# Optimization experiments

Hardware: AMD Instinct MI355X
Metric: run time of the kernel (lower is better)

## Reference

```python
import jax, jax.numpy as jnp
import numpy as np

B, T, C, H, WIN = 1, 2048, 512, 8, 48
DH = C // H  # 64


def setup_inputs() -> dict:
    key = jax.random.key(0)
    kx, kq, ko, kp = jax.random.split(key, 4)
    x = jax.random.normal(kx, (B, T, C), dtype=jnp.float32)
    W_qkv = jax.random.normal(kq, (C, 3 * C), dtype=jnp.float32) / np.sqrt(C).astype(np.float32)
    W_out = jax.random.normal(ko, (C, C), dtype=jnp.float32) / np.sqrt(C).astype(np.float32)
    # one random cycle permutation per head: perms[h, pi_pos] = original_pos
    perms = jax.vmap(lambda k: jax.random.permutation(k, T))(jax.random.split(kp, H)).astype(jnp.int32)
    return {"x": x, "W_qkv": W_qkv, "W_out": W_out, "perms": perms}


def _head_attn(qh, kh, vh, perm):
    # qh, kh, vh: [B, T, DH]; perm: [T] with perm[pi_pos] = original_pos
    Tn = perm.shape[0]
    inv_perm = jnp.argsort(perm)  # inv_perm[orig_pos] = pi_pos
    q_pi = qh[:, perm]
    k_pi = kh[:, perm]
    v_pi = vh[:, perm]
    offs = jnp.arange(-WIN, WIN + 1)                      # [W]
    pi_idx = jnp.arange(Tn)[:, None] + offs[None, :]      # [T, W]
    idx = jnp.clip(pi_idx, 0, Tn - 1)
    k_win = k_pi[:, idx]                                  # [B, T, W, DH]
    v_win = v_pi[:, idx]                                  # [B, T, W, DH]
    scores = jnp.einsum('btd,btwd->btw', q_pi, k_win) / np.sqrt(DH).astype(np.float32)
    neigh_orig = perm[idx]                                # [T, W] original positions of neighbors
    mask = (neigh_orig <= perm[:, None]) & (pi_idx >= 0) & (pi_idx < Tn)  # causal + window validity
    scores = jnp.where(mask[None], scores, jnp.finfo(scores.dtype).min)
    w = jax.nn.softmax(scores, axis=-1)                   # [B, T, W]
    y_pi = jnp.einsum('btw,btwd->btd', w, v_win)          # [B, T, DH]
    return y_pi[:, inv_perm]                              # back to original order


def reference(x, W_qkv, W_out, perms):
    qkv = x @ W_qkv                                       # [B, T, 3C]
    q, k, v = jnp.split(qkv, 3, axis=-1)
    q = q.reshape(B, T, H, DH)
    k = k.reshape(B, T, H, DH)
    v = v.reshape(B, T, H, DH)
    # heads are independent; vmap over head axis with per-head permutation
    y = jax.vmap(_head_attn, in_axes=(2, 2, 2, 0), out_axes=2)(q, k, v, perms)  # [B, T, H, DH]
    return y.reshape(B, T, C) @ W_out
```

## Files before the change

kernel.cpp:

```cpp
#include <hip/hip_runtime.h>
#include <float.h>
#include <math.h>

#define T_DIM 2048
#define C_DIM 512
#define QKV_LD 1536
#define NBLK 512

typedef float f32x4 __attribute__((ext_vector_type(4)));
typedef short s16x8 __attribute__((ext_vector_type(8)));

__device__ __forceinline__ unsigned short f2bf(float f) {
  unsigned u = __float_as_uint(f);
  return (unsigned short)((u + 0x7fffu + ((u >> 16) & 1u)) >> 16);
}

__device__ __forceinline__ void load16_to_lds(const void* g, void* l) {
  __builtin_amdgcn_global_load_lds(
      (const __attribute__((address_space(1))) unsigned int*)g,
      (__attribute__((address_space(3))) unsigned int*)(unsigned int)(unsigned long long)l,
      16, 0, 0);
}

template <int BM, bool AF32, bool OUT16>
__device__ __forceinline__ void gemm_body(const void* __restrict__ Ap,
                                          const float* __restrict__ B,
                                          void* __restrict__ Cp,
                                          int N, int K, int tilesX,
                                          unsigned short* lA, unsigned short* lB,
                                          int tid, int bid) {
  constexpr int BK = 32;
  constexpr int BM2 = BM / 2, BN2 = 32;
  constexpr int MT = BM2 / 16, NT = 2;
  const int lane = tid & 63, w = tid >> 6, wr = w >> 1, wc = w & 1;
  const int fm = lane & 15, q4 = lane >> 4, q8 = q4 * 8;

  const int m0 = (bid / tilesX) * BM, n0 = (bid % tilesX) * 64;
  const int bn = lane;
  const int bslot = w ^ ((bn >> 1) & 3);

  f32x4 acc[MT][NT] = {};
  for (int k0 = 0; k0 < K; k0 += BK) {
    __syncthreads();
    if constexpr (AF32) {
      const float* A = (const float*)Ap;
#pragma unroll
      for (int i = 0; i < BM / 64; ++i) {
        int c = i * 256 + tid;
        int row = c >> 2, c8 = (c & 3) * 8;
        const float* src = &A[(size_t)(m0 + row) * K + k0 + c8];
        float4 v0 = *(const float4*)src;
        float4 v1 = *(const float4*)(src + 4);
        uint4 o;
        o.x = f2bf(v0.x) | ((unsigned)f2bf(v0.y) << 16);
        o.y = f2bf(v0.z) | ((unsigned)f2bf(v0.w) << 16);
        o.z = f2bf(v1.x) | ((unsigned)f2bf(v1.y) << 16);
        o.w = f2bf(v1.z) | ((unsigned)f2bf(v1.w) << 16);
        *(uint4*)(lA + row * 32 + c8) = o;
      }
    } else {
      const unsigned short* A = (const unsigned short*)Ap;
#pragma unroll
      for (int i = 0; i < BM / 64; ++i) {
        int c = i * 256 + tid, row = c >> 2, c8 = (c & 3) * 8;
        load16_to_lds(&A[(size_t)(m0 + row) * K + k0 + c8], lA + c * 8);
      }
    }
    {
      float f[8];
#pragma unroll
      for (int i = 0; i < 8; ++i)
        f[i] = B[(size_t)(k0 + w * 8 + i) * N + n0 + bn];
      uint4 o;
      o.x = f2bf(f[0]) | ((unsigned)f2bf(f[1]) << 16);
      o.y = f2bf(f[2]) | ((unsigned)f2bf(f[3]) << 16);
      o.z = f2bf(f[4]) | ((unsigned)f2bf(f[5]) << 16);
      o.w = f2bf(f[6]) | ((unsigned)f2bf(f[7]) << 16);
      *(uint4*)(lB + bn * 32 + bslot * 8) = o;
    }
    __syncthreads();
    s16x8 a[MT], b[NT];
#pragma unroll
    for (int mi = 0; mi < MT; ++mi)
      a[mi] = *(const s16x8*)&lA[(wr * BM2 + mi * 16 + fm) * BK + q8];
#pragma unroll
    for (int ni = 0; ni < NT; ++ni) {
      int row = wc * BN2 + ni * 16 + fm;
      b[ni] = *(const s16x8*)&lB[row * 32 + ((q4 ^ ((row >> 1) & 3)) * 8)];
    }
#pragma unroll
    for (int mi = 0; mi < MT; ++mi)
#pragma unroll
      for (int ni = 0; ni < NT; ++ni)
        acc[mi][ni] = __builtin_amdgcn_mfma_f32_16x16x32_bf16(a[mi], b[ni], acc[mi][ni], 0, 0, 0);
  }
#pragma unroll
  for (int mi = 0; mi < MT; ++mi)
#pragma unroll
    for (int ni = 0; ni < NT; ++ni)
#pragma unroll
      for (int r = 0; r < 4; ++r) {
        int row = m0 + wr * BM2 + mi * 16 + q4 * 4 + r;
        int col = n0 + wc * BN2 + ni * 16 + fm;
        if constexpr (OUT16)
          ((unsigned short*)Cp)[(size_t)row * N + col] = f2bf(acc[mi][ni][r]);
        else
          ((float*)Cp)[(size_t)row * N + col] = acc[mi][ni][r];
      }
}

__global__ __launch_bounds__(256) void gemm1_kernel(const float* __restrict__ x,
                                                    const float* __restrict__ Wqkv,
                                                    unsigned short* __restrict__ qkvbf) {
  __shared__ __align__(16) unsigned short smem[(128 + 64) * 32];
  gemm_body<128, true, true>(x, Wqkv, qkvbf, QKV_LD, C_DIM, 24,
                             smem, smem + 128 * 32, threadIdx.x, blockIdx.x);
}
__global__ __launch_bounds__(256) void gemm2_kernel(const unsigned short* __restrict__ Ybf,
                                                    const float* __restrict__ Wout,
                                                    float* __restrict__ out) {
  __shared__ __align__(16) unsigned short smem[(64 + 64) * 32];
  gemm_body<64, false, false>(Ybf, Wout, out, C_DIM, C_DIM, 8,
                              smem, smem + 64 * 32, threadIdx.x, blockIdx.x);
}

__global__ __launch_bounds__(256) void attn_kernel(const unsigned short* __restrict__ qkvbf,
                                                   const int* __restrict__ perms,
                                                   unsigned short* __restrict__ Ybf) {
  __shared__ __align__(16) unsigned char smem[48768];
  int* ow            = (int*)smem;
  unsigned short* lQ = (unsigned short*)(smem + 512);
  unsigned short* lK = (unsigned short*)(smem + 5120);
  float* Sb          = (float*)(smem + 23552);
  unsigned short* lP = (unsigned short*)(smem + 40064);
  unsigned short* lVT= (unsigned short*)(smem + 5120);

  const int tid = threadIdx.x, bid = blockIdx.x;
  const int lane = tid & 63, w = tid >> 6;
  const int fm = lane & 15, q8 = (lane >> 4) * 8, q4 = lane >> 4;
  const int h = bid >> 6;
  const int t0 = (bid & 63) << 5;

  if (tid < 128) {
    int pi = t0 - 48 + tid;
    int idx = min(max(pi, 0), T_DIM - 1);
    ow[tid] = perms[h * T_DIM + idx];
  }
  __syncthreads();

#pragma unroll
  for (int it = 0; it < 4; ++it) {
    int c = it * 256 + tid;
    int row = c >> 3, k8 = c & 7;
    uint4 d = *(const uint4*)(qkvbf + (size_t)ow[row] * QKV_LD + C_DIM + h * 64 + k8 * 8);
    *(uint4*)(lK + row * 72 + k8 * 8) = d;
  }
  {
    int row = tid >> 3, k8 = tid & 7;
    uint4 d = *(const uint4*)(qkvbf + (size_t)ow[48 + row] * QKV_LD + h * 64 + k8 * 8);
    *(uint4*)(lQ + row * 72 + k8 * 8) = d;
  }
  __syncthreads();

  {
    f32x4 accs[2][2] = {};
#pragma unroll
    for (int kt = 0; kt < 2; ++kt) {
      s16x8 aq[2];
#pragma unroll
      for (int mi = 0; mi < 2; ++mi)
        aq[mi] = *(const s16x8*)&lQ[(mi * 16 + fm) * 72 + kt * 32 + q8];
#pragma unroll
      for (int ni = 0; ni < 2; ++ni) {
        s16x8 bk = *(const s16x8*)&lK[(w * 32 + ni * 16 + fm) * 72 + kt * 32 + q8];
#pragma unroll
        for (int mi = 0; mi < 2; ++mi)
          accs[mi][ni] = __builtin_amdgcn_mfma_f32_16x16x32_bf16(aq[mi], bk, accs[mi][ni], 0, 0, 0);
      }
    }
#pragma unroll
    for (int mi = 0; mi < 2; ++mi)
#pragma unroll
      for (int ni = 0; ni < 2; ++ni)
#pragma unroll
        for (int r = 0; r < 4; ++r)
          Sb[(mi * 16 + q4 * 4 + r) * 129 + w * 32 + ni * 16 + fm] = accs[mi][ni][r] * 0.125f;
  }
  __syncthreads();

#pragma unroll
  for (int it = 0; it < 4; ++it) {
    int c = it * 256 + tid;
    int j = c >> 3, d0 = (c & 7) * 8;
    uint4 v = *(const uint4*)(qkvbf + (size_t)ow[j] * QKV_LD + 2 * C_DIM + h * 64 + d0);
    lVT[(d0 + 0) * 136 + j] = (unsigned short)(v.x & 0xffff);
    lVT[(d0 + 1) * 136 + j] = (unsigned short)(v.x >> 16);
    lVT[(d0 + 2) * 136 + j] = (unsigned short)(v.y & 0xffff);
    lVT[(d0 + 3) * 136 + j] = (unsigned short)(v.y >> 16);
    lVT[(d0 + 4) * 136 + j] = (unsigned short)(v.z & 0xffff);
    lVT[(d0 + 5) * 136 + j] = (unsigned short)(v.z >> 16);
    lVT[(d0 + 6) * 136 + j] = (unsigned short)(v.w & 0xffff);
    lVT[(d0 + 7) * 136 + j] = (unsigned short)(v.w >> 16);
  }

  for (int si = 0; si < 8; ++si) {
    const int s = w * 8 + si;
    const int p = ow[48 + s];
    const int c1 = lane + 64;
    const float v0 = Sb[s * 129 + lane];
    const float v1 = Sb[s * 129 + c1];
    const int pi0 = t0 - 48 + lane;
    const bool valid0 = (lane >= s) && (pi0 >= 0) && (pi0 < T_DIM) && (ow[lane] <= p);
    const bool valid1 = (lane <= s + 32) && (pi0 + 64 < T_DIM) && (ow[c1] <= p);
    float mx = fmaxf(valid0 ? v0 : -FLT_MAX, valid1 ? v1 : -FLT_MAX);
#pragma unroll
    for (int off = 32; off > 0; off >>= 1) mx = fmaxf(mx, __shfl_xor(mx, off, 64));
    const float e0 = valid0 ? __expf(v0 - mx) : 0.f;
    const float e1 = valid1 ? __expf(v1 - mx) : 0.f;
    float sum = e0 + e1;
#pragma unroll
    for (int off = 32; off > 0; off >>= 1) sum += __shfl_xor(sum, off, 64);
    const float inv = 1.f / sum;
    lP[s * 136 + lane] = valid0 ? f2bf(e0 * inv) : (unsigned short)0;
    lP[s * 136 + c1]   = valid1 ? f2bf(e1 * inv) : (unsigned short)0;
  }
  __syncthreads();

  {
    const int wr = w >> 1, wc = w & 1;
    f32x4 acco[2] = {};
#pragma unroll
    for (int kt = 0; kt < 4; ++kt) {
      s16x8 ap = *(const s16x8*)&lP[(wr * 16 + fm) * 136 + kt * 32 + q8];
#pragma unroll
      for (int ni = 0; ni < 2; ++ni) {
        s16x8 bv = *(const s16x8*)&lVT[((wc * 2 + ni) * 16 + fm) * 136 + kt * 32 + q8];
        acco[ni] = __builtin_amdgcn_mfma_f32_16x16x32_bf16(ap, bv, acco[ni], 0, 0, 0);
      }
    }
#pragma unroll
    for (int ni = 0; ni < 2; ++ni)
#pragma unroll
      for (int r = 0; r < 4; ++r) {
        int q = wr * 16 + q4 * 4 + r;
        int d = (wc * 2 + ni) * 16 + fm;
        Ybf[(size_t)ow[48 + q] * C_DIM + h * 64 + d] = f2bf(acco[ni][r]);
      }
  }
}

extern "C" void kernel_launch(void* const* d_in, const int* in_sizes, int n_in,
                              void* d_out, int out_size, void* d_ws, size_t ws_size,
                              hipStream_t stream) {
  const float* x     = (const float*)d_in[0];
  const float* Wqkv  = (const float*)d_in[1];
  const float* Wout  = (const float*)d_in[2];
  const int*   perms = (const int*)d_in[3];
  float* out = (float*)d_out;
  unsigned short* ws = (unsigned short*)d_ws;

  unsigned short* qkvbf = ws;
  unsigned short* Ybf   = qkvbf + 3145728;

  gemm1_kernel<<<384, 256, 0, stream>>>(x, Wqkv, qkvbf);
  attn_kernel<<<NBLK, 256, 0, stream>>>(qkvbf, perms, Ybf);
  gemm2_kernel<<<256, 256, 0, stream>>>(Ybf, Wout, out);
}
```

Baseline: 104.6 us.

## Stage full weight K-panel in LDS once and prefetch A in GEMMs

Both GEMM kernels now convert the whole 512-deep bf16 B panel for their 64 output columns into LDS up front, using an XOR swizzle, rather than reloading and converting a 32-row slice every K step. gemm1 also prefetches the next fp32 A tile into registers while the current tile is in use. Separately, the attention V-transpose staging packs pairs of rows into 32-bit LDS stores, halving the number of scattered 16-bit writes. The cost is 64KB of LDS per GEMM block, which lowers occupancy, plus a long serial prologue before the first MFMA.

```diff
diff --git a/kernel.cpp b/kernel.cpp
--- a/kernel.cpp
+++ b/kernel.cpp
@@ -22,106 +22,140 @@
       16, 0, 0);
 }
 
-template <int BM, bool AF32, bool OUT16>
-__device__ __forceinline__ void gemm_body(const void* __restrict__ Ap,
-                                          const float* __restrict__ B,
-                                          void* __restrict__ Cp,
-                                          int N, int K, int tilesX,
-                                          unsigned short* lA, unsigned short* lB,
-                                          int tid, int bid) {
-  constexpr int BK = 32;
-  constexpr int BM2 = BM / 2, BN2 = 32;
-  constexpr int MT = BM2 / 16, NT = 2;
-  const int lane = tid & 63, w = tid >> 6, wr = w >> 1, wc = w & 1;
-  const int fm = lane & 15, q4 = lane >> 4, q8 = q4 * 8;
-
-  const int m0 = (bid / tilesX) * BM, n0 = (bid % tilesX) * 64;
-  const int bn = lane;
-  const int bslot = w ^ ((bn >> 1) & 3);
-
-  f32x4 acc[MT][NT] = {};
-  for (int k0 = 0; k0 < K; k0 += BK) {
-    __syncthreads();
-    if constexpr (AF32) {
-      const float* A = (const float*)Ap;
-#pragma unroll
-      for (int i = 0; i < BM / 64; ++i) {
-        int c = i * 256 + tid;
-        int row = c >> 2, c8 = (c & 3) * 8;
-        const float* src = &A[(size_t)(m0 + row) * K + k0 + c8];
-        float4 v0 = *(const float4*)src;
-        float4 v1 = *(const float4*)(src + 4);
-        uint4 o;
-        o.x = f2bf(v0.x) | ((unsigned)f2bf(v0.y) << 16);
-        o.y = f2bf(v0.z) | ((unsigned)f2bf(v0.w) << 16);
-        o.z = f2bf(v1.x) | ((unsigned)f2bf(v1.y) << 16);
-        o.w = f2bf(v1.z) | ((unsigned)f2bf(v1.w) << 16);
-        *(uint4*)(lA + row * 32 + c8) = o;
-      }
-    } else {
-      const unsigned short* A = (const unsigned short*)Ap;
-#pragma unroll
-      for (int i = 0; i < BM / 64; ++i) {
-        int c = i * 256 + tid, row = c >> 2, c8 = (c & 3) * 8;
-        load16_to_lds(&A[(size_t)(m0 + row) * K + k0 + c8], lA + c * 8);
-      }
-    }
-    {
-      float f[8];
-#pragma unroll
-      for (int i = 0; i < 8; ++i)
-        f[i] = B[(size_t)(k0 + w * 8 + i) * N + n0 + bn];
-      uint4 o;
-      o.x = f2bf(f[0]) | ((unsigned)f2bf(f[1]) << 16);
-      o.y = f2bf(f[2]) | ((unsigned)f2bf(f[3]) << 16);
-      o.z = f2bf(f[4]) | ((unsigned)f2bf(f[5]) << 16);
-      o.w = f2bf(f[6]) | ((unsigned)f2bf(f[7]) << 16);
-      *(uint4*)(lB + bn * 32 + bslot * 8) = o;
-    }
-    __syncthreads();
-    s16x8 a[MT], b[NT];
-#pragma unroll
-    for (int mi = 0; mi < MT; ++mi)
-      a[mi] = *(const s16x8*)&lA[(wr * BM2 + mi * 16 + fm) * BK + q8];
-#pragma unroll
-    for (int ni = 0; ni < NT; ++ni) {
-      int row = wc * BN2 + ni * 16 + fm;
-      b[ni] = *(const s16x8*)&lB[row * 32 + ((q4 ^ ((row >> 1) & 3)) * 8)];
-    }
-#pragma unroll
-    for (int mi = 0; mi < MT; ++mi)
-#pragma unroll
-      for (int ni = 0; ni < NT; ++ni)
-        acc[mi][ni] = __builtin_amdgcn_mfma_f32_16x16x32_bf16(a[mi], b[ni], acc[mi][ni], 0, 0, 0);
-  }
-#pragma unroll
-  for (int mi = 0; mi < MT; ++mi)
-#pragma unroll
-    for (int ni = 0; ni < NT; ++ni)
-#pragma unroll
-      for (int r = 0; r < 4; ++r) {
-        int row = m0 + wr * BM2 + mi * 16 + q4 * 4 + r;
-        int col = n0 + wc * BN2 + ni * 16 + fm;
-        if constexpr (OUT16)
-          ((unsigned short*)Cp)[(size_t)row * N + col] = f2bf(acc[mi][ni][r]);
-        else
-          ((float*)Cp)[(size_t)row * N + col] = acc[mi][ni][r];
-      }
+__device__ __forceinline__ void stage_B_panel(const float* __restrict__ W, int ldw,
+                                              int n0, unsigned short* lB,
+                                              int lane, int w) {
+  const int n = n0 + lane;
+#pragma unroll
+  for (int ko = 0; ko < 16; ++ko) {
+    const int chunk = ko * 4 + w;
+    const int kbase = chunk * 8;
+    float f[8];
+#pragma unroll
+    for (int j = 0; j < 8; ++j)
+      f[j] = W[(size_t)(kbase + j) * ldw + n];
+    uint4 o;
+    o.x = f2bf(f[0]) | ((unsigned)f2bf(f[1]) << 16);
+    o.y = f2bf(f[2]) | ((unsigned)f2bf(f[3]) << 16);
+    o.z = f2bf(f[4]) | ((unsigned)f2bf(f[5]) << 16);
+    o.w = f2bf(f[6]) | ((unsigned)f2bf(f[7]) << 16);
+    const int slot = chunk ^ (lane & 7);
+    *(uint4*)(lB + lane * 512 + slot * 8) = o;
+  }
 }
 
 __global__ __launch_bounds__(256) void gemm1_kernel(const float* __restrict__ x,
                                                     const float* __restrict__ Wqkv,
                                                     unsigned short* __restrict__ qkvbf) {
-  __shared__ __align__(16) unsigned short smem[(128 + 64) * 32];
-  gemm_body<128, true, true>(x, Wqkv, qkvbf, QKV_LD, C_DIM, 24,
-                             smem, smem + 128 * 32, threadIdx.x, blockIdx.x);
-}
+  __shared__ __align__(16) unsigned short lB[64 * 512];
+  __shared__ __align__(16) unsigned short lA[128 * 32];
+  const int tid = threadIdx.x, bid = blockIdx.x;
+  const int lane = tid & 63, w = tid >> 6, wr = w >> 1, wc = w & 1;
+  const int fm = lane & 15, q4 = lane >> 4, q8 = q4 * 8;
+  const int m0 = (bid / 24) * 128, n0 = (bid % 24) * 64;
+
+  stage_B_panel(Wqkv, QKV_LD, n0, lB, lane, w);
+
+  const int a_row = tid >> 2, a_c8 = (tid & 3) * 8;
+  const int a_row2 = a_row + 64;
+  float4 g[4];
+  auto loadA = [&](int kk) {
+    const float* s0 = &x[(size_t)(m0 + a_row) * C_DIM + kk + a_c8];
+    const float* s1 = &x[(size_t)(m0 + a_row2) * C_DIM + kk + a_c8];
+    g[0] = *(const float4*)s0; g[1] = *(const float4*)(s0 + 4);
+    g[2] = *(const float4*)s1; g[3] = *(const float4*)(s1 + 4);
+  };
+  loadA(0);
+
+  f32x4 acc[4][2] = {};
+  for (int i = 0; i < 16; ++i) {
+    __syncthreads();
+#pragma unroll
+    for (int ii = 0; ii < 2; ++ii) {
+      float4 v0 = g[ii * 2], v1 = g[ii * 2 + 1];
+      uint4 o;
+      o.x = f2bf(v0.x) | ((unsigned)f2bf(v0.y) << 16);
+      o.y = f2bf(v0.z) | ((unsigned)f2bf(v0.w) << 16);
+      o.z = f2bf(v1.x) | ((unsigned)f2bf(v1.y) << 16);
+      o.w = f2bf(v1.z) | ((unsigned)f2bf(v1.w) << 16);
+      *(uint4*)(lA + (ii ? a_row2 : a_row) * 32 + a_c8) = o;
+    }
+    __syncthreads();
+    if (i < 15) loadA((i + 1) * 32);
+
+    s16x8 a[4], b[2];
+#pragma unroll
+    for (int mi = 0; mi < 4; ++mi)
+      a[mi] = *(const s16x8*)&lA[(wr * 64 + mi * 16 + fm) * 32 + q8];
+#pragma unroll
+    for (int ni = 0; ni < 2; ++ni) {
+      int n = wc * 32 + ni * 16 + fm;
+      int slot = (i * 4 + q4) ^ (n & 7);
+      b[ni] = *(const s16x8*)&lB[n * 512 + slot * 8];
+    }
+#pragma unroll
+    for (int mi = 0; mi < 4; ++mi)
+#pragma unroll
+      for (int ni = 0; ni < 2; ++ni)
+        acc[mi][ni] = __builtin_amdgcn_mfma_f32_16x16x32_bf16(a[mi], b[ni], acc[mi][ni], 0, 0, 0);
+  }
+#pragma unroll
+  for (int mi = 0; mi < 4; ++mi)
+#pragma unroll
+    for (int ni = 0; ni < 2; ++ni)
+#pragma unroll
+      for (int r = 0; r < 4; ++r) {
+        int row = m0 + wr * 64 + mi * 16 + q4 * 4 + r;
+        int col = n0 + wc * 32 + ni * 16 + fm;
+        qkvbf[(size_t)row * QKV_LD + col] = f2bf(acc[mi][ni][r]);
+      }
+}
+
 __global__ __launch_bounds__(256) void gemm2_kernel(const unsigned short* __restrict__ Ybf,
                                                     const float* __restrict__ Wout,
                                                     float* __restrict__ out) {
-  __shared__ __align__(16) unsigned short smem[(64 + 64) * 32];
-  gemm_body<64, false, false>(Ybf, Wout, out, C_DIM, C_DIM, 8,
-                              smem, smem + 64 * 32, threadIdx.x, blockIdx.x);
+  __shared__ __align__(16) unsigned short lB[64 * 512];
+  __shared__ __align__(16) unsigned short lA[64 * 32];
+  const int tid = threadIdx.x, bid = blockIdx.x;
+  const int lane = tid & 63, w = tid >> 6, wr = w >> 1, wc = w & 1;
+  const int fm = lane & 15, q4 = lane >> 4, q8 = q4 * 8;
+  const int m0 = (bid / 8) * 64, n0 = (bid % 8) * 64;
+
+  stage_B_panel(Wout, C_DIM, n0, lB, lane, w);
+
+  const int a_row = tid >> 2, a_c8 = (tid & 3) * 8;
+  f32x4 acc[2][2] = {};
+  for (int i = 0; i < 16; ++i) {
+    __syncthreads();
+    load16_to_lds(&Ybf[(size_t)(m0 + a_row) * C_DIM + i * 32 + a_c8], lA + tid * 8);
+    __syncthreads();
+
+    s16x8 a[2], b[2];
+#pragma unroll
+    for (int mi = 0; mi < 2; ++mi)
+      a[mi] = *(const s16x8*)&lA[(wr * 32 + mi * 16 + fm) * 32 + q8];
+#pragma unroll
+    for (int ni = 0; ni < 2; ++ni) {
+      int n = wc * 32 + ni * 16 + fm;
+      int slot = (i * 4 + q4) ^ (n & 7);
+      b[ni] = *(const s16x8*)&lB[n * 512 + slot * 8];
+    }
+#pragma unroll
+    for (int mi = 0; mi < 2; ++mi)
+#pragma unroll
+      for (int ni = 0; ni < 2; ++ni)
+        acc[mi][ni] = __builtin_amdgcn_mfma_f32_16x16x32_bf16(a[mi], b[ni], acc[mi][ni], 0, 0, 0);
+  }
+#pragma unroll
+  for (int mi = 0; mi < 2; ++mi)
+#pragma unroll
+    for (int ni = 0; ni < 2; ++ni)
+#pragma unroll
+      for (int r = 0; r < 4; ++r) {
+        int row = m0 + wr * 32 + mi * 16 + q4 * 4 + r;
+        int col = n0 + wc * 32 + ni * 16 + fm;
+        out[(size_t)row * C_DIM + col] = acc[mi][ni][r];
+      }
 }
 
 __global__ __launch_bounds__(256) void attn_kernel(const unsigned short* __restrict__ qkvbf,
@@ -189,18 +223,19 @@
   __syncthreads();
 
 #pragma unroll
-  for (int it = 0; it < 4; ++it) {
-    int c = it * 256 + tid;
-    int j = c >> 3, d0 = (c & 7) * 8;
-    uint4 v = *(const uint4*)(qkvbf + (size_t)ow[j] * QKV_LD + 2 * C_DIM + h * 64 + d0);
-    lVT[(d0 + 0) * 136 + j] = (unsigned short)(v.x & 0xffff);
-    lVT[(d0 + 1) * 136 + j] = (unsigned short)(v.x >> 16);
-    lVT[(d0 + 2) * 136 + j] = (unsigned short)(v.y & 0xffff);
-    lVT[(d0 + 3) * 136 + j] = (unsigned short)(v.y >> 16);
-    lVT[(d0 + 4) * 136 + j] = (unsigned short)(v.z & 0xffff);
-    lVT[(d0 + 5) * 136 + j] = (unsigned short)(v.z >> 16);
-    lVT[(d0 + 6) * 136 + j] = (unsigned short)(v.w & 0xffff);
-    lVT[(d0 + 7) * 136 + j] = (unsigned short)(v.w >> 16);
+  for (int it = 0; it < 2; ++it) {
+    int c2 = it * 256 + tid;
+    int r = c2 & 63, d0 = (c2 >> 6) * 8;
+    uint4 va = *(const uint4*)(qkvbf + (size_t)ow[2 * r]     * QKV_LD + 2 * C_DIM + h * 64 + d0);
+    uint4 vb = *(const uint4*)(qkvbf + (size_t)ow[2 * r + 1] * QKV_LD + 2 * C_DIM + h * 64 + d0);
+    *(unsigned*)(lVT + (d0 + 0) * 136 + 2 * r) = (va.x & 0xffffu) | (vb.x << 16);
+    *(unsigned*)(lVT + (d0 + 1) * 136 + 2 * r) = (va.x >> 16) | (vb.x & 0xffff0000u);
+    *(unsigned*)(lVT + (d0 + 2) * 136 + 2 * r) = (va.y & 0xffffu) | (vb.y << 16);
+    *(unsigned*)(lVT + (d0 + 3) * 136 + 2 * r) = (va.y >> 16) | (vb.y & 0xffff0000u);
+    *(unsigned*)(lVT + (d0 + 4) * 136 + 2 * r) = (va.z & 0xffffu) | (vb.z << 16);
+    *(unsigned*)(lVT + (d0 + 5) * 136 + 2 * r) = (va.z >> 16) | (vb.z & 0xffff0000u);
+    *(unsigned*)(lVT + (d0 + 6) * 136 + 2 * r) = (va.w & 0xffffu) | (vb.w << 16);
+    *(unsigned*)(lVT + (d0 + 7) * 136 + 2 * r) = (va.w >> 16) | (vb.w & 0xffff0000u);
   }
 
   for (int si = 0; si < 8; ++si) {
```

Result: faster. 99.75 us (-4.6%).
